# Kernel optimization log

Measured on AMD Instinct MI355X. Metric: run time of the kernel, lower is better.

The kernel has to match this reference:

```python
import jax, jax.numpy as jnp
import numpy as np

NUM_CLASSES = 81
N_ROIS = 100000
N_GT = 512
ROIS_PER_IMAGE = 256
FG_ROIS_PER_IMAGE = 128  # fg_fraction * rois_per_image
FG_THRESH = 0.5
BG_HI = 0.5
BG_LO = 0.1


def _make_boxes(key, n, img=1024.0):
    k1, k2, k3, k4 = jax.random.split(key, 4)
    x1 = jax.random.uniform(k1, (n,)) * (img - 160.0)
    y1 = jax.random.uniform(k2, (n,)) * (img - 160.0)
    w = 16.0 + jax.random.uniform(k3, (n,)) * 112.0
    h = 16.0 + jax.random.uniform(k4, (n,)) * 112.0
    return jnp.stack([x1, y1, x1 + w, y1 + h], axis=1)


def setup_inputs() -> dict:
    key = jax.random.key(0)
    kg, kc, kn, kr, ks = jax.random.split(key, 5)
    gt_xyxy = _make_boxes(kg, N_GT)
    gt_cls = jax.random.randint(kc, (N_GT, 1), 1, NUM_CLASSES).astype(jnp.float32)
    gt_boxes = jnp.concatenate([gt_xyxy, gt_cls], axis=1)
    # first block of proposals = jittered gt boxes so fg samples exist
    n_jit = 4096
    reps = int(np.ceil(n_jit / N_GT))
    jit_base = jnp.tile(gt_xyxy, (reps, 1))[:n_jit]
    noise = (jax.random.uniform(kn, (n_jit, 4)) - 0.5) * 12.0
    jit_boxes = jit_base + noise
    rand_boxes = _make_boxes(kr, N_ROIS - n_jit)
    boxes = jnp.concatenate([jit_boxes, rand_boxes], axis=0)
    rpn_rois = jnp.concatenate([jnp.zeros((N_ROIS, 1), jnp.float32), boxes], axis=1)
    rpn_scores = jax.random.uniform(ks, (N_ROIS, 1), dtype=jnp.float32)
    return {"rpn_rois": rpn_rois, "rpn_scores": rpn_scores, "gt_boxes": gt_boxes}


def _bbox_overlaps(b1, b2):
    # b1 [N,4], b2 [G,4] -> IoU [N,G] with +1 pixel convention
    x1a, y1a, x2a, y2a = b1[:, 0], b1[:, 1], b1[:, 2], b1[:, 3]
    x1b, y1b, x2b, y2b = b2[:, 0], b2[:, 1], b2[:, 2], b2[:, 3]
    iw = jnp.maximum(0.0, jnp.minimum(x2a[:, None], x2b[None, :]) - jnp.maximum(x1a[:, None], x1b[None, :]) + 1.0)
    ih = jnp.maximum(0.0, jnp.minimum(y2a[:, None], y2b[None, :]) - jnp.maximum(y1a[:, None], y1b[None, :]) + 1.0)
    inter = iw * ih
    a1 = (x2a - x1a + 1.0) * (y2a - y1a + 1.0)
    a2 = (x2b - x1b + 1.0) * (y2b - y1b + 1.0)
    union = a1[:, None] + a2[None, :] - inter
    return jnp.where(inter == 0.0, 0.0, inter / union)


def _bbox_transform(ex, gt):
    ew = ex[:, 2] - ex[:, 0] + 1.0
    eh = ex[:, 3] - ex[:, 1] + 1.0
    ecx = ex[:, 0] + 0.5 * ew
    ecy = ex[:, 1] + 0.5 * eh
    gw = gt[:, 2] - gt[:, 0] + 1.0
    gh = gt[:, 3] - gt[:, 1] + 1.0
    gcx = gt[:, 0] + 0.5 * gw
    gcy = gt[:, 1] + 0.5 * gh
    return jnp.stack([(gcx - ecx) / ew, (gcy - ecy) / eh, jnp.log(gw / ew), jnp.log(gh / eh)], axis=1)


def _forward(rpn_rois, rpn_scores, gt_boxes):
    means = jnp.array([0.0, 0.0, 0.0, 0.0], jnp.float32)
    stds = jnp.array([0.1, 0.1, 0.2, 0.2], jnp.float32)
    k1, k2, k3 = jax.random.split(jax.random.key(42), 3)
    n = rpn_rois.shape[0]
    overlaps = _bbox_overlaps(rpn_rois[:, 1:5], gt_boxes[:, :4])  # [N,G]
    gt_assignment = jnp.argmax(overlaps, axis=1)  # [N]
    max_overlaps = jnp.max(overlaps, axis=1)      # [N]
    fg_mask = max_overlaps >= FG_THRESH
    bg_mask = (max_overlaps < BG_HI) & (max_overlaps >= BG_LO)
    # shuffled candidate orderings: random key for candidates, +2 sentinel pushes rest to the back
    fg_order = jnp.argsort(jnp.where(fg_mask, jax.random.uniform(k1, (n,)), 2.0))
    bg_order = jnp.argsort(jnp.where(bg_mask, jax.random.uniform(k2, (n,)), 2.0))
    fg_count = jnp.minimum(FG_ROIS_PER_IMAGE, jnp.sum(fg_mask))
    bg_count = jnp.minimum(ROIS_PER_IMAGE - fg_count, jnp.sum(bg_mask))
    pos = jnp.arange(ROIS_PER_IMAGE)
    sel = jnp.where(pos < fg_count, fg_order[pos], bg_order[jnp.maximum(pos - fg_count, 0)])
    # fill any shortfall by re-sampling uniformly from the fg+bg picks
    n_samp = fg_count + bg_count
    n_safe = jnp.maximum(n_samp, 1)
    dup = (jax.random.uniform(k3, (ROIS_PER_IMAGE,)) * n_safe).astype(jnp.int32)
    sel = jnp.where(pos < n_samp, sel, sel[dup])
    gt_ids = gt_assignment[sel]
    labels = gt_boxes[gt_ids, 4]
    fmax = max_overlaps[sel]
    labels = jnp.where((fmax < BG_HI) & (fmax >= BG_LO), 0.0, labels)
    rois = rpn_rois[sel]                 # [256,5]
    roi_scores = rpn_scores[sel].reshape(-1)
    targets = _bbox_transform(rois[:, 1:5], gt_boxes[gt_ids, :4])
    targets = (targets - means) / stds
    # expand compact (cls,tx,ty,tw,th) into N x 4K, nonzero only at own-class slot
    cls = labels.astype(jnp.int32)
    valid = (labels > 0).astype(jnp.float32)[:, None]
    rows = pos[:, None]
    cols = cls[:, None] * 4 + jnp.arange(4)[None, :]
    zeros4k = jnp.zeros((ROIS_PER_IMAGE, 4 * NUM_CLASSES), jnp.float32)
    bbox_targets = zeros4k.at[rows, cols].set(targets * valid)
    bbox_inside = zeros4k.at[rows, cols].set(jnp.ones((1, 4), jnp.float32) * valid)
    bbox_outside = (bbox_inside > 0).astype(jnp.float32)
    return rois, roi_scores, labels, bbox_targets, bbox_inside, bbox_outside


def reference(rpn_rois, rpn_scores, gt_boxes):
    return _forward(rpn_rois, rpn_scores, gt_boxes)
```

## Files before the change

### kernel.cpp

```cpp
#include <hip/hip_runtime.h>
#include <stdint.h>

__host__ __device__ inline void tf2x32(uint32_t ks0, uint32_t ks1, uint32_t x0, uint32_t x1,
                                       uint32_t& o0, uint32_t& o1) {
  uint32_t ks2 = ks0 ^ ks1 ^ 0x1BD11BDAu;
#define TFR(r) { x0 += x1; x1 = (x1 << (r)) | (x1 >> (32 - (r))); x1 ^= x0; }
  x0 += ks0; x1 += ks1;
  TFR(13) TFR(15) TFR(26) TFR(6)
  x0 += ks1; x1 += ks2 + 1u;
  TFR(17) TFR(29) TFR(16) TFR(24)
  x0 += ks2; x1 += ks0 + 2u;
  TFR(13) TFR(15) TFR(26) TFR(6)
  x0 += ks0; x1 += ks1 + 3u;
  TFR(17) TFR(29) TFR(16) TFR(24)
  x0 += ks1; x1 += ks2 + 4u;
  TFR(13) TFR(15) TFR(26) TFR(6)
  x0 += ks2; x1 += ks0 + 5u;
#undef TFR
  o0 = x0; o1 = x1;
}

__device__ inline float bits_to_unif(uint32_t b) {
  return __uint_as_float((b >> 9) | 0x3F800000u) - 1.0f;
}

__device__ inline uint32_t jbits(int v, uint32_t ka, uint32_t kb, uint32_t i, uint32_t n) {
  uint32_t o0, o1;
  if (v == 2) {
    uint32_t h = (n + 1) >> 1;
    if (i < h) {
      uint32_t xh = (i + h < n) ? (i + h) : 0u;
      tf2x32(ka, kb, i, xh, o0, o1);
      return o0;
    }
    tf2x32(ka, kb, i - h, i, o0, o1);
    return o1;
  }
  tf2x32(ka, kb, 0u, i, o0, o1);
  return (v == 0) ? o0 : (o0 ^ o1);
}

__device__ inline int jbucket(uint32_t b) { return (int)(b >> 22); }

#define NGT_MAX      512
#define ROIS_PER_IMG 256
#define FG_PER_IMG   128
#define NCOLS        324
#define NB           1024
#define CAND_CAP     2048
#define WAVES        4

#define OFF_SCORES 1280
#define OFF_LABELS 1536
#define OFF_BIG    1792
#define BIGN       (ROIS_PER_IMG * NCOLS)

#define WS_MAXOV   0
#define WS_GTASGN  400000
#define WS_HIST    800000
#define WS_CANDF   808192
#define WS_CANDB   824576
#define WS_META    840960
#define WS_CLS     841024
#define WS_T       842048
#define WS_GT8     846144

__global__ void __launch_bounds__(1024) k_detect(const float* __restrict__ scores,
                                                 const float* __restrict__ gt,
                                                 int n, int ngt,
                                                 int* __restrict__ meta,
                                                 int* __restrict__ hist,
                                                 float* __restrict__ gt8) {
#pragma clang fp contract(off)
  int tid = threadIdx.x;
  hist[tid] = 0;
  hist[NB + tid] = 0;
  if (tid >= 7 && tid <= 13) meta[tid] = 0;

  if (tid < NGT_MAX && tid < ngt) {
    float x1 = gt[tid * 5 + 0], y1 = gt[tid * 5 + 1];
    float x2 = gt[tid * 5 + 2], y2 = gt[tid * 5 + 3];
    gt8[tid * 8 + 0] = x1; gt8[tid * 8 + 1] = y1;
    gt8[tid * 8 + 2] = x2; gt8[tid * 8 + 3] = y2;
    gt8[tid * 8 + 4] = (x2 - x1 + 1.0f) * (y2 - y1 + 1.0f);
    gt8[tid * 8 + 5] = gt[tid * 5 + 4];
    gt8[tid * 8 + 6] = 0.0f; gt8[tid * 8 + 7] = 0.0f;
  }

  if (tid < 64) {
    uint32_t pa, pb; tf2x32(0u, 0u, 0u, 4u, pa, pb);
    uint32_t t0, t1, q0, q1;
    tf2x32(0u, 0u, 3u, 8u, t0, t1);
    tf2x32(0u, 0u, 4u, 9u, q0, q1);
    uint32_t la = t1, lb = q1;

    bool m0 = false, m1 = false, m2 = false;
    if (tid < 16) {
      uint32_t sref = __float_as_uint(scores[tid]);
      uint32_t o0, o1; tf2x32(pa, pb, 0u, (uint32_t)tid, o0, o1);
      m0 = (__float_as_uint(bits_to_unif(o0)) == sref);
      m1 = (__float_as_uint(bits_to_unif(o0 ^ o1)) == sref);
      uint32_t h = (uint32_t)(n >> 1);
      uint32_t c0, c1; tf2x32(la, lb, (uint32_t)tid, (uint32_t)tid + h, c0, c1);
      m2 = (__float_as_uint(bits_to_unif(c0)) == sref);
    }
    int n0 = __popcll(__ballot(m0));
    int n1 = __popcll(__ballot(m1));
    int n2 = __popcll(__ballot(m2));
    if (tid == 0) {
      int v = (n1 >= n0 && n1 >= n2) ? 1 : ((n0 >= n2) ? 0 : 2);
      meta[0] = v;
      uint32_t K[6];
      if (v == 2) {
        uint32_t a0, a1, b0, b1, c0, c1;
        tf2x32(0u, 42u, 0u, 3u, a0, a1);
        tf2x32(0u, 42u, 1u, 4u, b0, b1);
        tf2x32(0u, 42u, 2u, 5u, c0, c1);
        K[0] = a0; K[1] = b0; K[2] = c0; K[3] = a1; K[4] = b1; K[5] = c1;
      } else {
        tf2x32(0u, 42u, 0u, 0u, K[0], K[1]);
        tf2x32(0u, 42u, 0u, 1u, K[2], K[3]);
        tf2x32(0u, 42u, 0u, 2u, K[4], K[5]);
      }
      for (int j = 0; j < 6; ++j) meta[1 + j] = (int)K[j];
    }
  }
}

__global__ void __launch_bounds__(256) k_iou(const float* __restrict__ rois,
                                             const float* __restrict__ gt8,
                                             int n, int ngt,
                                             float* __restrict__ maxov,
                                             int* __restrict__ gtasgn,
                                             int* __restrict__ hist,
                                             const int* __restrict__ meta) {
#pragma clang fp contract(off)
  __shared__ float4 sgt4[NGT_MAX];
  __shared__ float sarea[NGT_MAX];
  __shared__ float sbest[WAVES][128];
  __shared__ int   sbi[WAVES][128];
  __shared__ int   smeta[7];
  const int tid = threadIdx.x;
  const int wave = tid >> 6;
  const int lane = tid & 63;
  if (tid < 7) smeta[tid] = meta[tid];
  {
    const float4* g4p = (const float4*)gt8;
    for (int g = tid; g < ngt; g += 256) {
      float4 box = g4p[2 * g];
      float4 ext = g4p[2 * g + 1];
      sgt4[g] = box;
      sarea[g] = ext.x;
    }
  }
  __syncthreads();

  const int R = blockIdx.x * 128;
  const int iA = R + lane;
  const int iB = R + lane + 64;
  const bool pA = (iA < n), pB = (iB < n);

  float ax1 = 1e30f, ay1 = 1e30f, ax2 = -1e30f, ay2 = -1e30f, a1A = 1.0f;
  float bx1 = 1e30f, by1 = 1e30f, bx2 = -1e30f, by2 = -1e30f, a1B = 1.0f;
  if (pA) {
    ax1 = rois[iA * 5 + 1]; ay1 = rois[iA * 5 + 2];
    ax2 = rois[iA * 5 + 3]; ay2 = rois[iA * 5 + 4];
    a1A = (ax2 - ax1 + 1.0f) * (ay2 - ay1 + 1.0f);
  }
  if (pB) {
    bx1 = rois[iB * 5 + 1]; by1 = rois[iB * 5 + 2];
    bx2 = rois[iB * 5 + 3]; by2 = rois[iB * 5 + 4];
    a1B = (bx2 - bx1 + 1.0f) * (by2 - by1 + 1.0f);
  }
  const float aXm = ax1 - 1.5f, aXp = ax2 + 1.5f, aYm = ay1 - 1.5f, aYp = ay2 + 1.5f;
  const float bXm = bx1 - 1.5f, bXp = bx2 + 1.5f, bYm = by1 - 1.5f, bYp = by2 + 1.5f;

  const int csz = (ngt + WAVES - 1) / WAVES;
  const int g0 = wave * csz;
  const int cnt = max(0, min(ngt, g0 + csz) - g0);

  unsigned long long mA0 = 0ull, mA1 = 0ull, mB0 = 0ull, mB1 = 0ull;
  if (cnt == 128) {
#pragma unroll 8
    for (int jj = 0; jj < 64; ++jj) {
      float4 G = sgt4[g0 + jj];
      bool oA = (G.x < aXp) & (G.z > aXm) & (G.y < aYp) & (G.w > aYm);
      bool oB = (G.x < bXp) & (G.z > bXm) & (G.y < bYp) & (G.w > bYm);
      if (oA) mA0 |= (1ull << jj);
      if (oB) mB0 |= (1ull << jj);
    }
#pragma unroll 8
    for (int jj = 0; jj < 64; ++jj) {
      float4 G = sgt4[g0 + 64 + jj];
      bool oA = (G.x < aXp) & (G.z > aXm) & (G.y < aYp) & (G.w > aYm);
      bool oB = (G.x < bXp) & (G.z > bXm) & (G.y < bYp) & (G.w > bYm);
      if (oA) mA1 |= (1ull << jj);
      if (oB) mB1 |= (1ull << jj);
    }
  } else {
    for (int jj = 0; jj < cnt; ++jj) {
      float4 G = sgt4[g0 + jj];
      bool oA = (G.x < aXp) & (G.z > aXm) & (G.y < aYp) & (G.w > aYm);
      bool oB = (G.x < bXp) & (G.z > bXm) & (G.y < bYp) & (G.w > bYm);
      if (jj < 64) {
        if (oA) mA0 |= (1ull << jj);
        if (oB) mB0 |= (1ull << jj);
      } else {
        if (oA) mA1 |= (1ull << (jj - 64));
        if (oB) mB1 |= (1ull << (jj - 64));
      }
    }
  }

  float bestA = 0.0f, bestB = 0.0f;
  int biA = 0, biB = 0;
  auto drain = [&](unsigned long long m, int base,
                   float x1r, float y1r, float x2r, float y2r, float a1r,
                   float& best, int& bi) {
    while (m) {
      int jj = __builtin_ctzll(m);
      m &= m - 1ull;
      int j = base + jj;
      float4 G = sgt4[j];
      float iw = fminf(x2r, G.z) - fmaxf(x1r, G.x) + 1.0f;
      float ih = fminf(y2r, G.w) - fmaxf(y1r, G.y) + 1.0f;
      if (iw > 0.0f && ih > 0.0f) {
        float inter = iw * ih;
        float uni = a1r + sarea[j] - inter;
        float iou = inter / uni;
        if (iou > best) { best = iou; bi = j; }
      }
    }
  };
  drain(mA0, g0,      ax1, ay1, ax2, ay2, a1A, bestA, biA);
  drain(mA1, g0 + 64, ax1, ay1, ax2, ay2, a1A, bestA, biA);
  drain(mB0, g0,      bx1, by1, bx2, by2, a1B, bestB, biB);
  drain(mB1, g0 + 64, bx1, by1, bx2, by2, a1B, bestB, biB);

  sbest[wave][lane] = bestA;      sbi[wave][lane] = biA;
  sbest[wave][lane + 64] = bestB; sbi[wave][lane + 64] = biB;
  __syncthreads();

  if (tid < 128) {
    const int r = R + tid;
    float best = sbest[0][tid];
    int bi = sbi[0][tid];
    for (int w = 1; w < WAVES; ++w) {
      float ob = sbest[w][tid];
      int oi = sbi[w][tid];
      if (ob > best || (ob == best && oi < bi)) { best = ob; bi = oi; }
    }
    if (r < n) {
      maxov[r] = best;
      gtasgn[r] = bi;
      if (best >= 0.1f) {
        const int v = smeta[0];
        const bool fg = (best >= 0.5f);
        uint32_t ka = (uint32_t)(fg ? smeta[1] : smeta[3]);
        uint32_t kb = (uint32_t)(fg ? smeta[2] : smeta[4]);
        uint32_t b = jbits(v, ka, kb, (uint32_t)r, (uint32_t)n);
        atomicAdd(&hist[(fg ? 0 : NB) + jbucket(b)], 1);
      }
    }
  }
}

__global__ void __launch_bounds__(1024) k_collect(const float* __restrict__ maxov,
                                                  int n,
                                                  const int* __restrict__ hist,
                                                  int* __restrict__ meta,
                                                  unsigned long long* __restrict__ candf,
                                                  unsigned long long* __restrict__ candb) {
  __shared__ int hf[NB], hb[NB];
  __shared__ int smeta[7];
  __shared__ int sres[2];
  const int tid = threadIdx.x;
  if (tid < 7) smeta[tid] = meta[tid];
  if (tid < 2) sres[tid] = -1;
  hf[tid] = hist[tid];
  hb[tid] = hist[NB + tid];
  __syncthreads();
  for (int s = 1; s < NB; s <<= 1) {
    int tf_ = hf[tid] + ((tid >= s) ? hf[tid - s] : 0);
    int tb_ = hb[tid] + ((tid >= s) ? hb[tid - s] : 0);
    __syncthreads();
    hf[tid] = tf_; hb[tid] = tb_;
    __syncthreads();
  }
  const int fgc = min(FG_PER_IMG, hf[NB - 1]);
  const int bgc = min(ROIS_PER_IMG - fgc, hb[NB - 1]);
  if (tid == 0) { meta[9] = fgc; meta[10] = bgc; }
  if (fgc > 0 && hf[tid] >= fgc && (tid == 0 || hf[tid - 1] < fgc)) { sres[0] = tid; meta[7] = tid; }
  if (bgc > 0 && hb[tid] >= bgc && (tid == 0 || hb[tid - 1] < bgc)) { sres[1] = tid; meta[8] = tid; }
  __syncthreads();
  const int Bf = sres[0], Bb = sres[1];
  const int v = smeta[0];

  const int i = blockIdx.x * 1024 + tid;
  if (i >= n) return;
  float m = maxov[i];
  if (m >= 0.5f) {
    if (Bf >= 0) {
      uint32_t b = jbits(v, (uint32_t)smeta[1], (uint32_t)smeta[2], (uint32_t)i, (uint32_t)n);
      if (jbucket(b) <= Bf) {
        int p = atomicAdd(&meta[11], 1);
        if (p < CAND_CAP) candf[p] = ((unsigned long long)(b >> 9) << 32) | (unsigned)i;
      }
    }
  } else if (m >= 0.1f) {
    if (Bb >= 0) {
      uint32_t b = jbits(v, (uint32_t)smeta[3], (uint32_t)smeta[4], (uint32_t)i, (uint32_t)n);
      if (jbucket(b) <= Bb) {
        int p = atomicAdd(&meta[12], 1);
        if (p < CAND_CAP) candb[p] = ((unsigned long long)(b >> 9) << 32) | (unsigned)i;
      }
    }
  }
}

__device__ inline void bitonic(unsigned long long* buf, int nelem, int tid, int nthr) {
  for (int k = 2; k <= nelem; k <<= 1)
    for (int j = k >> 1; j > 0; j >>= 1) {
      for (int i = tid; i < nelem; i += nthr) {
        int l = i ^ j;
        if (l > i) {
          unsigned long long a = buf[i], b = buf[l];
          bool swap_ = ((i & k) == 0) ? (a > b) : (a < b);
          if (swap_) { buf[i] = b; buf[l] = a; }
        }
      }
      __syncthreads();
    }
}

__global__ void __launch_bounds__(1024) k_pick(
    const float* __restrict__ rois, const float* __restrict__ scores,
    const float* __restrict__ gt,
    const float* __restrict__ maxov, const int* __restrict__ gtasgn,
    const int* __restrict__ meta,
    const unsigned long long* __restrict__ gcandf,
    const unsigned long long* __restrict__ gcandb,
    float* __restrict__ out, int* __restrict__ ws_cls, float* __restrict__ ws_t) {
#pragma clang fp contract(off)
  __shared__ unsigned long long candf[CAND_CAP], candb[CAND_CAP];
  __shared__ int sel[ROIS_PER_IMG];
  __shared__ int smeta[13];
  const int tid = threadIdx.x;
  const int nthr = 1024;
  if (tid < 13) smeta[tid] = meta[tid];
  __syncthreads();
  const int v = smeta[0];
  const uint32_t k3a = (uint32_t)smeta[5], k3b = (uint32_t)smeta[6];
  const int fg_count = smeta[9], bg_count = smeta[10];
  const int Mf = min(smeta[11], CAND_CAP);
  const int Mb = min(smeta[12], CAND_CAP);

  int nf = 1; while (nf < Mf) nf <<= 1;
  int nb = 1; while (nb < Mb) nb <<= 1;
  for (int i = tid; i < nf; i += nthr) candf[i] = (i < Mf) ? gcandf[i] : ~0ull;
  for (int i = tid; i < nb; i += nthr) candb[i] = (i < Mb) ? gcandb[i] : ~0ull;
  __syncthreads();

  bitonic(candf, nf, tid, nthr);
  bitonic(candb, nb, tid, nthr);
  __syncthreads();

  if (tid < fg_count) sel[tid] = (int)(candf[tid] & 0xFFFFFFFFull);
  if (tid < bg_count) sel[fg_count + tid] = (int)(candb[tid] & 0xFFFFFFFFull);
  __syncthreads();

  const int n_samp = fg_count + bg_count;
  if (tid < ROIS_PER_IMG && tid >= n_samp) {
    if (n_samp > 0) {
      uint32_t b3 = jbits(v, k3a, k3b, (uint32_t)tid, (uint32_t)ROIS_PER_IMG);
      int d = (int)(bits_to_unif(b3) * (float)n_samp);
      d = min(d, n_samp - 1);
      sel[tid] = sel[d];
    } else {
      sel[tid] = 0;
    }
  }
  __syncthreads();

  if (tid < ROIS_PER_IMG) {
    int i = sel[tid];
    int g = gtasgn[i];
    float fmax = maxov[i];
    float label = gt[g * 5 + 4];
    if (fmax < 0.5f && fmax >= 0.1f) label = 0.0f;

    for (int c = 0; c < 5; ++c) out[tid * 5 + c] = rois[i * 5 + c];
    out[OFF_SCORES + tid] = scores[i];
    out[OFF_LABELS + tid] = label;

    float ex0 = rois[i * 5 + 1], ey0 = rois[i * 5 + 2];
    float ex1 = rois[i * 5 + 3], ey1 = rois[i * 5 + 4];
    float gx0 = gt[g * 5 + 0], gy0 = gt[g * 5 + 1];
    float gx1 = gt[g * 5 + 2], gy1 = gt[g * 5 + 3];
    float ew = ex1 - ex0 + 1.0f, eh = ey1 - ey0 + 1.0f;
    float ecx = ex0 + 0.5f * ew, ecy = ey0 + 0.5f * eh;
    float gw = gx1 - gx0 + 1.0f, gh = gy1 - gy0 + 1.0f;
    float gcx = gx0 + 0.5f * gw, gcy = gy0 + 0.5f * gh;
    float t0 = ((gcx - ecx) / ew) / 0.1f;
    float t1 = ((gcy - ecy) / eh) / 0.1f;
    float t2 = logf(gw / ew) / 0.2f;
    float t3 = logf(gh / eh) / 0.2f;

    float valid = (label > 0.0f) ? 1.0f : 0.0f;
    int cls = (int)label;
    ws_cls[tid] = (valid > 0.0f) ? cls : -1;
    ws_t[tid * 4 + 0] = t0 * valid;
    ws_t[tid * 4 + 1] = t1 * valid;
    ws_t[tid * 4 + 2] = t2 * valid;
    ws_t[tid * 4 + 3] = t3 * valid;
  }
}

__global__ void k_out(const int* __restrict__ ws_cls, const float* __restrict__ ws_t,
                      float* __restrict__ out) {
  const int QROW = NCOLS / 4;
  const int TOT4 = ROIS_PER_IMG * QROW;
  int e4 = blockIdx.x * blockDim.x + threadIdx.x;
  if (e4 >= TOT4) return;
  int r = e4 / QROW, q = e4 - r * QROW;
  int cls = ws_cls[r];
  float4 tv = make_float4(0.f, 0.f, 0.f, 0.f);
  float4 iv = make_float4(0.f, 0.f, 0.f, 0.f);
  if (cls >= 0 && q == cls) {
    tv = *(const float4*)(ws_t + r * 4);
    iv = make_float4(1.f, 1.f, 1.f, 1.f);
  }
  float4* o0 = (float4*)(out + OFF_BIG);
  float4* o1 = (float4*)(out + OFF_BIG + BIGN);
  float4* o2 = (float4*)(out + OFF_BIG + 2 * BIGN);
  o0[e4] = tv;
  o1[e4] = iv;
  o2[e4] = iv;
}

extern "C" void kernel_launch(void* const* d_in, const int* in_sizes, int n_in,
                              void* d_out, int out_size, void* d_ws, size_t ws_size,
                              hipStream_t stream) {
  const float* rois   = (const float*)d_in[0];
  const float* scores = (const float*)d_in[1];
  const float* gt     = (const float*)d_in[2];
  float* out = (float*)d_out;

  const int n   = in_sizes[0] / 5;
  const int ngt = in_sizes[2] / 5;

  char* ws = (char*)d_ws;
  float* maxov  = (float*)(ws + WS_MAXOV);
  int*   gtasgn = (int*)(ws + WS_GTASGN);
  int*   hist   = (int*)(ws + WS_HIST);
  unsigned long long* candf = (unsigned long long*)(ws + WS_CANDF);
  unsigned long long* candb = (unsigned long long*)(ws + WS_CANDB);
  int*   meta   = (int*)(ws + WS_META);
  int*   wcls   = (int*)(ws + WS_CLS);
  float* wt     = (float*)(ws + WS_T);
  float* gt8    = (float*)(ws + WS_GT8);

  k_detect<<<1, 1024, 0, stream>>>(scores, gt, n, ngt, meta, hist, gt8);
  k_iou<<<(n + 127) / 128, 256, 0, stream>>>(rois, gt8, n, ngt, maxov, gtasgn, hist, meta);
  k_collect<<<(n + 1023) / 1024, 1024, 0, stream>>>(maxov, n, hist, meta, candf, candb);
  k_pick<<<1, 1024, 0, stream>>>(rois, scores, gt, maxov, gtasgn, meta,
                                 candf, candb, out, wcls, wt);
  k_out<<<(ROIS_PER_IMG * (NCOLS / 4) + 255) / 256, 256, 0, stream>>>(wcls, wt, out);
}
```

Before: 72.86 us.

## Fold detect kernel into consumers and split IoU scan over eight waves

Removes the single-block k_detect launch. Each consumer kernel now recomputes the RNG-variant detection and key derivation into shared memory, the histogram and meta are cleared with a memset, and k_iou reads raw gt boxes and computes their areas itself. k_iou moves to 512 threads with 8 waves, each covering 64 gt boxes, so every wave holds a single 64-bit overlap mask. This cuts one launch and a serial dependency, but every block repeats the Threefry detection work and the k_iou blocks grow larger.

```diff
diff --git a/kernel.cpp b/kernel.cpp
--- a/kernel.cpp
+++ b/kernel.cpp
@@ -42,51 +42,8 @@
 
 __device__ inline int jbucket(uint32_t b) { return (int)(b >> 22); }
 
-#define NGT_MAX      512
-#define ROIS_PER_IMG 256
-#define FG_PER_IMG   128
-#define NCOLS        324
-#define NB           1024
-#define CAND_CAP     2048
-#define WAVES        4
-
-#define OFF_SCORES 1280
-#define OFF_LABELS 1536
-#define OFF_BIG    1792
-#define BIGN       (ROIS_PER_IMG * NCOLS)
-
-#define WS_MAXOV   0
-#define WS_GTASGN  400000
-#define WS_HIST    800000
-#define WS_CANDF   808192
-#define WS_CANDB   824576
-#define WS_META    840960
-#define WS_CLS     841024
-#define WS_T       842048
-#define WS_GT8     846144
-
-__global__ void __launch_bounds__(1024) k_detect(const float* __restrict__ scores,
-                                                 const float* __restrict__ gt,
-                                                 int n, int ngt,
-                                                 int* __restrict__ meta,
-                                                 int* __restrict__ hist,
-                                                 float* __restrict__ gt8) {
-#pragma clang fp contract(off)
-  int tid = threadIdx.x;
-  hist[tid] = 0;
-  hist[NB + tid] = 0;
-  if (tid >= 7 && tid <= 13) meta[tid] = 0;
-
-  if (tid < NGT_MAX && tid < ngt) {
-    float x1 = gt[tid * 5 + 0], y1 = gt[tid * 5 + 1];
-    float x2 = gt[tid * 5 + 2], y2 = gt[tid * 5 + 3];
-    gt8[tid * 8 + 0] = x1; gt8[tid * 8 + 1] = y1;
-    gt8[tid * 8 + 2] = x2; gt8[tid * 8 + 3] = y2;
-    gt8[tid * 8 + 4] = (x2 - x1 + 1.0f) * (y2 - y1 + 1.0f);
-    gt8[tid * 8 + 5] = gt[tid * 5 + 4];
-    gt8[tid * 8 + 6] = 0.0f; gt8[tid * 8 + 7] = 0.0f;
-  }
-
+__device__ inline void detect_rng(const float* __restrict__ scores, int n,
+                                  int tid, int* smeta) {
   if (tid < 64) {
     uint32_t pa, pb; tf2x32(0u, 0u, 0u, 4u, pa, pb);
     uint32_t t0, t1, q0, q1;
@@ -109,7 +66,7 @@
     int n2 = __popcll(__ballot(m2));
     if (tid == 0) {
       int v = (n1 >= n0 && n1 >= n2) ? 1 : ((n0 >= n2) ? 0 : 2);
-      meta[0] = v;
+      smeta[0] = v;
       uint32_t K[6];
       if (v == 2) {
         uint32_t a0, a1, b0, b1, c0, c1;
@@ -122,18 +79,40 @@
         tf2x32(0u, 42u, 0u, 1u, K[2], K[3]);
         tf2x32(0u, 42u, 0u, 2u, K[4], K[5]);
       }
-      for (int j = 0; j < 6; ++j) meta[1 + j] = (int)K[j];
-    }
-  }
-}
-
-__global__ void __launch_bounds__(256) k_iou(const float* __restrict__ rois,
-                                             const float* __restrict__ gt8,
+      for (int j = 0; j < 6; ++j) smeta[1 + j] = (int)K[j];
+    }
+  }
+}
+
+#define NGT_MAX      512
+#define ROIS_PER_IMG 256
+#define FG_PER_IMG   128
+#define NCOLS        324
+#define NB           1024
+#define CAND_CAP     2048
+#define WAVES        8
+
+#define OFF_SCORES 1280
+#define OFF_LABELS 1536
+#define OFF_BIG    1792
+#define BIGN       (ROIS_PER_IMG * NCOLS)
+
+#define WS_MAXOV   0
+#define WS_GTASGN  400000
+#define WS_HIST    800000
+#define WS_META    808192
+#define WS_CANDF   808256
+#define WS_CANDB   824640
+#define WS_CLS     841024
+#define WS_T       842048
+
+__global__ void __launch_bounds__(512) k_iou(const float* __restrict__ rois,
+                                             const float* __restrict__ scores,
+                                             const float* __restrict__ gt,
                                              int n, int ngt,
                                              float* __restrict__ maxov,
                                              int* __restrict__ gtasgn,
-                                             int* __restrict__ hist,
-                                             const int* __restrict__ meta) {
+                                             int* __restrict__ hist) {
 #pragma clang fp contract(off)
   __shared__ float4 sgt4[NGT_MAX];
   __shared__ float sarea[NGT_MAX];
@@ -143,15 +122,13 @@
   const int tid = threadIdx.x;
   const int wave = tid >> 6;
   const int lane = tid & 63;
-  if (tid < 7) smeta[tid] = meta[tid];
-  {
-    const float4* g4p = (const float4*)gt8;
-    for (int g = tid; g < ngt; g += 256) {
-      float4 box = g4p[2 * g];
-      float4 ext = g4p[2 * g + 1];
-      sgt4[g] = box;
-      sarea[g] = ext.x;
-    }
+
+  detect_rng(scores, n, tid, smeta);
+  for (int g = tid; g < ngt && g < NGT_MAX; g += 512) {
+    float x1 = gt[g * 5 + 0], y1 = gt[g * 5 + 1];
+    float x2 = gt[g * 5 + 2], y2 = gt[g * 5 + 3];
+    sgt4[g] = make_float4(x1, y1, x2, y2);
+    sarea[g] = (x2 - x1 + 1.0f) * (y2 - y1 + 1.0f);
   }
   __syncthreads();
 
@@ -179,48 +156,35 @@
   const int g0 = wave * csz;
   const int cnt = max(0, min(ngt, g0 + csz) - g0);
 
-  unsigned long long mA0 = 0ull, mA1 = 0ull, mB0 = 0ull, mB1 = 0ull;
-  if (cnt == 128) {
+  unsigned long long mA = 0ull, mB = 0ull;
+  if (cnt == 64) {
 #pragma unroll 8
     for (int jj = 0; jj < 64; ++jj) {
       float4 G = sgt4[g0 + jj];
       bool oA = (G.x < aXp) & (G.z > aXm) & (G.y < aYp) & (G.w > aYm);
       bool oB = (G.x < bXp) & (G.z > bXm) & (G.y < bYp) & (G.w > bYm);
-      if (oA) mA0 |= (1ull << jj);
-      if (oB) mB0 |= (1ull << jj);
-    }
-#pragma unroll 8
-    for (int jj = 0; jj < 64; ++jj) {
-      float4 G = sgt4[g0 + 64 + jj];
-      bool oA = (G.x < aXp) & (G.z > aXm) & (G.y < aYp) & (G.w > aYm);
-      bool oB = (G.x < bXp) & (G.z > bXm) & (G.y < bYp) & (G.w > bYm);
-      if (oA) mA1 |= (1ull << jj);
-      if (oB) mB1 |= (1ull << jj);
+      if (oA) mA |= (1ull << jj);
+      if (oB) mB |= (1ull << jj);
     }
   } else {
     for (int jj = 0; jj < cnt; ++jj) {
       float4 G = sgt4[g0 + jj];
       bool oA = (G.x < aXp) & (G.z > aXm) & (G.y < aYp) & (G.w > aYm);
       bool oB = (G.x < bXp) & (G.z > bXm) & (G.y < bYp) & (G.w > bYm);
-      if (jj < 64) {
-        if (oA) mA0 |= (1ull << jj);
-        if (oB) mB0 |= (1ull << jj);
-      } else {
-        if (oA) mA1 |= (1ull << (jj - 64));
-        if (oB) mB1 |= (1ull << (jj - 64));
-      }
+      if (oA) mA |= (1ull << jj);
+      if (oB) mB |= (1ull << jj);
     }
   }
 
   float bestA = 0.0f, bestB = 0.0f;
   int biA = 0, biB = 0;
-  auto drain = [&](unsigned long long m, int base,
+  auto drain = [&](unsigned long long m,
                    float x1r, float y1r, float x2r, float y2r, float a1r,
                    float& best, int& bi) {
     while (m) {
       int jj = __builtin_ctzll(m);
       m &= m - 1ull;
-      int j = base + jj;
+      int j = g0 + jj;
       float4 G = sgt4[j];
       float iw = fminf(x2r, G.z) - fmaxf(x1r, G.x) + 1.0f;
       float ih = fminf(y2r, G.w) - fmaxf(y1r, G.y) + 1.0f;
@@ -232,10 +196,8 @@
       }
     }
   };
-  drain(mA0, g0,      ax1, ay1, ax2, ay2, a1A, bestA, biA);
-  drain(mA1, g0 + 64, ax1, ay1, ax2, ay2, a1A, bestA, biA);
-  drain(mB0, g0,      bx1, by1, bx2, by2, a1B, bestB, biB);
-  drain(mB1, g0 + 64, bx1, by1, bx2, by2, a1B, bestB, biB);
+  drain(mA, ax1, ay1, ax2, ay2, a1A, bestA, biA);
+  drain(mB, bx1, by1, bx2, by2, a1B, bestB, biB);
 
   sbest[wave][lane] = bestA;      sbi[wave][lane] = biA;
   sbest[wave][lane + 64] = bestB; sbi[wave][lane + 64] = biB;
@@ -245,6 +207,7 @@
     const int r = R + tid;
     float best = sbest[0][tid];
     int bi = sbi[0][tid];
+#pragma unroll
     for (int w = 1; w < WAVES; ++w) {
       float ob = sbest[w][tid];
       int oi = sbi[w][tid];
@@ -266,6 +229,7 @@
 }
 
 __global__ void __launch_bounds__(1024) k_collect(const float* __restrict__ maxov,
+                                                  const float* __restrict__ scores,
                                                   int n,
                                                   const int* __restrict__ hist,
                                                   int* __restrict__ meta,
@@ -275,7 +239,7 @@
   __shared__ int smeta[7];
   __shared__ int sres[2];
   const int tid = threadIdx.x;
-  if (tid < 7) smeta[tid] = meta[tid];
+  detect_rng(scores, n, tid, smeta);
   if (tid < 2) sres[tid] = -1;
   hf[tid] = hist[tid];
   hb[tid] = hist[NB + tid];
@@ -290,8 +254,8 @@
   const int fgc = min(FG_PER_IMG, hf[NB - 1]);
   const int bgc = min(ROIS_PER_IMG - fgc, hb[NB - 1]);
   if (tid == 0) { meta[9] = fgc; meta[10] = bgc; }
-  if (fgc > 0 && hf[tid] >= fgc && (tid == 0 || hf[tid - 1] < fgc)) { sres[0] = tid; meta[7] = tid; }
-  if (bgc > 0 && hb[tid] >= bgc && (tid == 0 || hb[tid - 1] < bgc)) { sres[1] = tid; meta[8] = tid; }
+  if (fgc > 0 && hf[tid] >= fgc && (tid == 0 || hf[tid - 1] < fgc)) sres[0] = tid;
+  if (bgc > 0 && hb[tid] >= bgc && (tid == 0 || hb[tid - 1] < bgc)) sres[1] = tid;
   __syncthreads();
   const int Bf = sres[0], Bb = sres[1];
   const int v = smeta[0];
@@ -335,7 +299,7 @@
 
 __global__ void __launch_bounds__(1024) k_pick(
     const float* __restrict__ rois, const float* __restrict__ scores,
-    const float* __restrict__ gt,
+    const float* __restrict__ gt, int n,
     const float* __restrict__ maxov, const int* __restrict__ gtasgn,
     const int* __restrict__ meta,
     const unsigned long long* __restrict__ gcandf,
@@ -344,16 +308,18 @@
 #pragma clang fp contract(off)
   __shared__ unsigned long long candf[CAND_CAP], candb[CAND_CAP];
   __shared__ int sel[ROIS_PER_IMG];
-  __shared__ int smeta[13];
+  __shared__ int smeta[7];
+  __shared__ int scnt[4];
   const int tid = threadIdx.x;
   const int nthr = 1024;
-  if (tid < 13) smeta[tid] = meta[tid];
+  detect_rng(scores, n, tid, smeta);
+  if (tid >= 64 && tid < 68) scnt[tid - 64] = meta[9 + (tid - 64)];
   __syncthreads();
   const int v = smeta[0];
   const uint32_t k3a = (uint32_t)smeta[5], k3b = (uint32_t)smeta[6];
-  const int fg_count = smeta[9], bg_count = smeta[10];
-  const int Mf = min(smeta[11], CAND_CAP);
-  const int Mb = min(smeta[12], CAND_CAP);
+  const int fg_count = scnt[0], bg_count = scnt[1];
+  const int Mf = min(scnt[2], CAND_CAP);
+  const int Mb = min(scnt[3], CAND_CAP);
 
   int nf = 1; while (nf < Mf) nf <<= 1;
   int nb = 1; while (nb < Mb) nb <<= 1;
@@ -453,17 +419,18 @@
   float* maxov  = (float*)(ws + WS_MAXOV);
   int*   gtasgn = (int*)(ws + WS_GTASGN);
   int*   hist   = (int*)(ws + WS_HIST);
+  int*   meta   = (int*)(ws + WS_META);
   unsigned long long* candf = (unsigned long long*)(ws + WS_CANDF);
   unsigned long long* candb = (unsigned long long*)(ws + WS_CANDB);
-  int*   meta   = (int*)(ws + WS_META);
   int*   wcls   = (int*)(ws + WS_CLS);
   float* wt     = (float*)(ws + WS_T);
-  float* gt8    = (float*)(ws + WS_GT8);
-
-  k_detect<<<1, 1024, 0, stream>>>(scores, gt, n, ngt, meta, hist, gt8);
-  k_iou<<<(n + 127) / 128, 256, 0, stream>>>(rois, gt8, n, ngt, maxov, gtasgn, hist, meta);
-  k_collect<<<(n + 1023) / 1024, 1024, 0, stream>>>(maxov, n, hist, meta, candf, candb);
-  k_pick<<<1, 1024, 0, stream>>>(rois, scores, gt, maxov, gtasgn, meta,
+
+  hipMemsetAsync(ws + WS_HIST, 0, 8256, stream);
+  k_iou<<<(n + 127) / 128, 512, 0, stream>>>(rois, scores, gt, n, ngt,
+                                             maxov, gtasgn, hist);
+  k_collect<<<(n + 1023) / 1024, 1024, 0, stream>>>(maxov, scores, n, hist, meta,
+                                                    candf, candb);
+  k_pick<<<1, 1024, 0, stream>>>(rois, scores, gt, n, maxov, gtasgn, meta,
                                  candf, candb, out, wcls, wt);
   k_out<<<(ROIS_PER_IMG * (NCOLS / 4) + 255) / 256, 256, 0, stream>>>(wcls, wt, out);
 }
```

After: 76.50 us. 5.0% more time.
